# Performance work log

Hardware: AMD Instinct MI355X
Metric: run time of the kernel (lower is better)

The kernel has to match this reference:

```python
import jax, jax.numpy as jnp
import numpy as np

D_MODEL = 2048
NUM_EXPERTS = 64
TOP_K = 2


def setup_inputs() -> dict:
    key = jax.random.key(0)
    kx, kw, kb = jax.random.split(key, 3)
    x = jax.random.normal(kx, (4, 4096, D_MODEL), dtype=jnp.float32)
    # nn.Linear(d_model, num_experts): weight [num_experts, d_model], bias [num_experts]
    bound = 1.0 / np.sqrt(D_MODEL)
    W = jax.random.uniform(kw, (NUM_EXPERTS, D_MODEL), minval=-bound, maxval=bound, dtype=jnp.float32)
    b = jax.random.uniform(kb, (NUM_EXPERTS,), minval=-bound, maxval=bound, dtype=jnp.float32)
    return {"x": x, "W": W, "b": b}


def reference(x, W, b):
    # Eval mode: no noise injection (self.training is False).
    logits = jnp.einsum('bsd,ed->bse', x, W) + b          # [B, S, E]
    raw_weights = jax.nn.softmax(logits, axis=-1)          # [B, S, E]
    top_k_weights, top_k_indices = jax.lax.top_k(raw_weights, TOP_K)  # [B, S, K]
    normalized = top_k_weights / jnp.sum(top_k_weights, axis=-1, keepdims=True)
    return normalized, top_k_indices
```

## Files before the change

kernel.cpp:

```cpp
#include <hip/hip_runtime.h>
#include <math.h>

#define DM 2048
#define NEXP 64
#define NTOK 16384
#define BT 32
#define NW 8
#define KSL (DM / NW)
#define NKS (KSL / 32)
#define NBLK (NTOK / BT)
#define WELEMS (NEXP * DM)

typedef __attribute__((ext_vector_type(8))) short short8;
typedef __attribute__((ext_vector_type(4))) float f32x4;

__device__ __forceinline__ void split3(float f, unsigned short& h,
                                       unsigned short& m, unsigned short& l) {
  unsigned u = __float_as_uint(f);
  unsigned rh = (u + 0x7FFFu + ((u >> 16) & 1u)) >> 16;
  h = (unsigned short)rh;
  float f1 = f - __uint_as_float(rh << 16);
  unsigned u1 = __float_as_uint(f1);
  unsigned rm = (u1 + 0x7FFFu + ((u1 >> 16) & 1u)) >> 16;
  m = (unsigned short)rm;
  float f2 = f1 - __uint_as_float(rm << 16);
  unsigned u2 = __float_as_uint(f2);
  l = (unsigned short)((u2 + 0x7FFFu + ((u2 >> 16) & 1u)) >> 16);
}

__global__ void convw_kernel(const float* __restrict__ W,
                             unsigned short* __restrict__ whi,
                             unsigned short* __restrict__ wmid,
                             unsigned short* __restrict__ wlo) {
  int i = blockIdx.x * 256 + threadIdx.x;
  unsigned short h, m, l;
  split3(W[i], h, m, l);
  whi[i] = h; wmid[i] = m; wlo[i] = l;
}

template <bool USE_WS>
__global__ __launch_bounds__(512, 2)
void router_mfma(const float* __restrict__ x, const float* __restrict__ W,
                 const float* __restrict__ bias,
                 const unsigned short* __restrict__ whi,
                 const unsigned short* __restrict__ wmid,
                 const unsigned short* __restrict__ wlo,
                 float* __restrict__ out) {
  const int lane = threadIdx.x & 63;
  const int wv = threadIdx.x >> 6;
  const int col = lane & 15;
  const int quad = lane >> 4;
  const int tok0 = blockIdx.x * BT;
  const int k0 = wv * KSL;

  __shared__ float part[NW][BT][NEXP];

  f32x4 acc[2][4];
#pragma unroll
  for (int ms = 0; ms < 2; ++ms)
#pragma unroll
    for (int nt = 0; nt < 4; ++nt) acc[ms][nt] = (f32x4){0.f, 0.f, 0.f, 0.f};

  for (int ks = 0; ks < NKS; ++ks) {
    const int k = k0 + ks * 32 + quad * 8;

    short8 ah[2], am[2], al[2];
#pragma unroll
    for (int ms = 0; ms < 2; ++ms) {
      const f32x4* ap = (const f32x4*)(x + (size_t)(tok0 + ms * 16 + col) * DM + k);
      f32x4 a0 = ap[0], a1 = ap[1];
      float av[8] = {a0.x, a0.y, a0.z, a0.w, a1.x, a1.y, a1.z, a1.w};
#pragma unroll
      for (int j = 0; j < 8; ++j) {
        unsigned short h, m, l;
        split3(av[j], h, m, l);
        ah[ms][j] = (short)h; am[ms][j] = (short)m; al[ms][j] = (short)l;
      }
    }

#pragma unroll
    for (int nt = 0; nt < 4; ++nt) {
      short8 bh, bm, bl;
      const size_t widx = (size_t)(nt * 16 + col) * DM + k;
      if (USE_WS) {
        bh = *(const short8*)(whi + widx);
        bm = *(const short8*)(wmid + widx);
        bl = *(const short8*)(wlo + widx);
      } else {
        const f32x4* wp = (const f32x4*)(W + widx);
        f32x4 w0 = wp[0], w1 = wp[1];
        float wvv[8] = {w0.x, w0.y, w0.z, w0.w, w1.x, w1.y, w1.z, w1.w};
#pragma unroll
        for (int j = 0; j < 8; ++j) {
          unsigned short h, m, l;
          split3(wvv[j], h, m, l);
          bh[j] = (short)h; bm[j] = (short)m; bl[j] = (short)l;
        }
      }
#pragma unroll
      for (int ms = 0; ms < 2; ++ms) {
        f32x4 c = acc[ms][nt];
        c = __builtin_amdgcn_mfma_f32_16x16x32_bf16(ah[ms], bh, c, 0, 0, 0);
        c = __builtin_amdgcn_mfma_f32_16x16x32_bf16(ah[ms], bm, c, 0, 0, 0);
        c = __builtin_amdgcn_mfma_f32_16x16x32_bf16(am[ms], bh, c, 0, 0, 0);
        c = __builtin_amdgcn_mfma_f32_16x16x32_bf16(ah[ms], bl, c, 0, 0, 0);
        c = __builtin_amdgcn_mfma_f32_16x16x32_bf16(al[ms], bh, c, 0, 0, 0);
        c = __builtin_amdgcn_mfma_f32_16x16x32_bf16(am[ms], bm, c, 0, 0, 0);
        acc[ms][nt] = c;
      }
    }
  }

#pragma unroll
  for (int ms = 0; ms < 2; ++ms)
#pragma unroll
    for (int nt = 0; nt < 4; ++nt)
#pragma unroll
      for (int r = 0; r < 4; ++r)
        part[wv][ms * 16 + quad * 4 + r][nt * 16 + col] = acc[ms][nt][r];
  __syncthreads();

  const float bl_ = bias[lane];
#pragma unroll
  for (int ti = 0; ti < 4; ++ti) {
    const int t = wv * 4 + ti;
    float v1 = bl_;
#pragma unroll
    for (int p = 0; p < NW; ++p) v1 += part[p][t][lane];
    int i1 = lane;
    float v2 = -INFINITY;
    int i2 = NEXP;
#pragma unroll
    for (int off = 32; off > 0; off >>= 1) {
      float ov1 = __shfl_xor(v1, off, 64);
      int   oi1 = __shfl_xor(i1, off, 64);
      float ov2 = __shfl_xor(v2, off, 64);
      int   oi2 = __shfl_xor(i2, off, 64);
      bool afirst = (v1 > ov1) || (v1 == ov1 && i1 < oi1);
      float w1v = afirst ? v1 : ov1;  int w1i = afirst ? i1 : oi1;
      float c1v = afirst ? v2 : ov2;  int c1i = afirst ? i2 : oi2;
      float c2v = afirst ? ov1 : v1;  int c2i = afirst ? oi1 : i1;
      bool sfirst = (c1v > c2v) || (c1v == c2v && c1i < c2i);
      v1 = w1v; i1 = w1i;
      v2 = sfirst ? c1v : c2v;
      i2 = sfirst ? c1i : c2i;
    }
    if (lane == 0) {
      const float ex = expf(v2 - v1);
      const float den = 1.f + ex;
      const int token = tok0 + t;
      *(float2*)(out + 2 * token) = make_float2(1.f / den, ex / den);
      *(float2*)(out + 2 * NTOK + 2 * token) =
          make_float2((float)i1, (float)i2);
    }
  }
}

extern "C" void kernel_launch(void* const* d_in, const int* in_sizes, int n_in,
                              void* d_out, int out_size, void* d_ws, size_t ws_size,
                              hipStream_t stream) {
  const float* x = (const float*)d_in[0];
  const float* W = (const float*)d_in[1];
  const float* b = (const float*)d_in[2];
  float* out = (float*)d_out;

  const size_t need = 3ull * WELEMS * sizeof(unsigned short);
  if (ws_size >= need) {
    unsigned short* whi = (unsigned short*)d_ws;
    unsigned short* wmid = whi + WELEMS;
    unsigned short* wlo = wmid + WELEMS;
    hipLaunchKernelGGL(convw_kernel, dim3(WELEMS / 256), dim3(256), 0, stream,
                       W, whi, wmid, wlo);
    hipLaunchKernelGGL((router_mfma<true>), dim3(NBLK), dim3(512), 0, stream,
                       x, W, b, whi, wmid, wlo, out);
  } else {
    hipLaunchKernelGGL((router_mfma<false>), dim3(NBLK), dim3(512), 0, stream,
                       x, W, b, nullptr, nullptr, nullptr, out);
  }
}
```

Baseline: 231.8 us.

## Split router into LDS-staged split-K GEMM plus separate top-2 reduce kernel

```diff
diff --git a/kernel.cpp b/kernel.cpp
--- a/kernel.cpp
+++ b/kernel.cpp
@@ -4,129 +4,164 @@
 #define DM 2048
 #define NEXP 64
 #define NTOK 16384
-#define BT 32
-#define NW 8
-#define KSL (DM / NW)
-#define NKS (KSL / 32)
-#define NBLK (NTOK / BT)
-#define WELEMS (NEXP * DM)
+#define NSLICE 8
+#define KSL (DM / NSLICE)
+#define KC 32
+#define NCH (KSL / KC)
+#define MB 128
+#define NBLK1 ((NTOK / MB) * NSLICE)
+#define WFRAG_BYTES (64 * 12 * 1024)
+#define PART_BYTES (NSLICE * NTOK * NEXP * 4)
 
 typedef __attribute__((ext_vector_type(8))) short short8;
 typedef __attribute__((ext_vector_type(4))) float f32x4;
 
-__device__ __forceinline__ void split3(float f, unsigned short& h,
-                                       unsigned short& m, unsigned short& l) {
+__device__ __forceinline__ void async16(void* lds, const void* g) {
+  __builtin_amdgcn_global_load_lds(
+      (const __attribute__((address_space(1))) unsigned int*)g,
+      (__attribute__((address_space(3))) unsigned int*)lds, 16, 0, 0);
+}
+
+__device__ __forceinline__ void split3t(float f, unsigned short& h,
+                                        unsigned short& m, unsigned short& l) {
   unsigned u = __float_as_uint(f);
-  unsigned rh = (u + 0x7FFFu + ((u >> 16) & 1u)) >> 16;
-  h = (unsigned short)rh;
-  float f1 = f - __uint_as_float(rh << 16);
+  h = (unsigned short)(u >> 16);
+  float f1 = f - __uint_as_float(u & 0xFFFF0000u);
   unsigned u1 = __float_as_uint(f1);
-  unsigned rm = (u1 + 0x7FFFu + ((u1 >> 16) & 1u)) >> 16;
-  m = (unsigned short)rm;
-  float f2 = f1 - __uint_as_float(rm << 16);
-  unsigned u2 = __float_as_uint(f2);
-  l = (unsigned short)((u2 + 0x7FFFu + ((u2 >> 16) & 1u)) >> 16);
+  m = (unsigned short)(u1 >> 16);
+  float f2 = f1 - __uint_as_float(u1 & 0xFFFF0000u);
+  l = (unsigned short)(__float_as_uint(f2) >> 16);
+}
+
+__device__ __forceinline__ void split8(const f32x4& a0, const f32x4& a1,
+                                       short8& h, short8& m, short8& l) {
+  float v[8] = {a0[0], a0[1], a0[2], a0[3], a1[0], a1[1], a1[2], a1[3]};
+#pragma unroll
+  for (int j = 0; j < 8; ++j) {
+    unsigned short hh, mm, ll;
+    split3t(v[j], hh, mm, ll);
+    h[j] = (short)hh; m[j] = (short)mm; l[j] = (short)ll;
+  }
 }
 
 __global__ void convw_kernel(const float* __restrict__ W,
-                             unsigned short* __restrict__ whi,
-                             unsigned short* __restrict__ wmid,
-                             unsigned short* __restrict__ wlo) {
-  int i = blockIdx.x * 256 + threadIdx.x;
-  unsigned short h, m, l;
-  split3(W[i], h, m, l);
-  whi[i] = h; wmid[i] = m; wlo[i] = l;
-}
-
-template <bool USE_WS>
-__global__ __launch_bounds__(512, 2)
-void router_mfma(const float* __restrict__ x, const float* __restrict__ W,
-                 const float* __restrict__ bias,
-                 const unsigned short* __restrict__ whi,
-                 const unsigned short* __restrict__ wmid,
-                 const unsigned short* __restrict__ wlo,
-                 float* __restrict__ out) {
+                             unsigned short* __restrict__ wfrag) {
+  const int kg = blockIdx.x;
+  const int lane = threadIdx.x & 63;
+  const int nt = threadIdx.x >> 6;
+  const int e = nt * 16 + (lane & 15);
+  const int kpos = kg * 32 + (lane >> 4) * 8;
+  const f32x4* wp = (const f32x4*)(W + (size_t)e * DM + kpos);
+  f32x4 w0 = wp[0], w1 = wp[1];
+  short8 h, m, l;
+  split8(w0, w1, h, m, l);
+  size_t base = ((size_t)(kg * 12 + nt) * 64 + lane) * 8;
+  *(short8*)(wfrag + base) = h;
+  *(short8*)(wfrag + base + (size_t)4 * 64 * 8) = m;
+  *(short8*)(wfrag + base + (size_t)8 * 64 * 8) = l;
+}
+
+__global__ __launch_bounds__(256, 4)
+void router_gemm(const float* __restrict__ x,
+                 const unsigned short* __restrict__ wfrag,
+                 float* __restrict__ part) {
   const int lane = threadIdx.x & 63;
   const int wv = threadIdx.x >> 6;
   const int col = lane & 15;
   const int quad = lane >> 4;
-  const int tok0 = blockIdx.x * BT;
-  const int k0 = wv * KSL;
-
-  __shared__ float part[NW][BT][NEXP];
+  const int tg = blockIdx.x & ((NTOK / MB) - 1);
+  const int s = blockIdx.x >> 7;
+  const int tok0 = tg * MB;
+
+  __shared__ __align__(16) float xs[MB][KC];
+  __shared__ __align__(16) unsigned short bs[12][64][8];
 
   f32x4 acc[2][4];
 #pragma unroll
-  for (int ms = 0; ms < 2; ++ms)
-#pragma unroll
-    for (int nt = 0; nt < 4; ++nt) acc[ms][nt] = (f32x4){0.f, 0.f, 0.f, 0.f};
-
-  for (int ks = 0; ks < NKS; ++ks) {
-    const int k = k0 + ks * 32 + quad * 8;
+  for (int mt = 0; mt < 2; ++mt)
+#pragma unroll
+    for (int nt = 0; nt < 4; ++nt) acc[mt][nt] = (f32x4){0.f, 0.f, 0.f, 0.f};
+
+  for (int c = 0; c < NCH; ++c) {
+    const int kc = s * KSL + c * KC;
+    const int kg = s * NCH + c;
+
+#pragma unroll
+    for (int i = 0; i < 4; ++i) {
+      const int r = wv * 32 + i * 8;
+      const int tr = r + (lane >> 3);
+      const int unit = (lane & 7) ^ ((lane >> 3) & 7);
+      async16(&xs[r][0],
+              x + (size_t)(tok0 + tr) * DM + kc + unit * 4);
+    }
+#pragma unroll
+    for (int q = 0; q < 3; ++q) {
+      const int m = wv * 3 + q;
+      async16(&bs[m][0][0],
+              wfrag + ((size_t)kg * 12 + m) * 512 + (size_t)lane * 8);
+    }
+    __syncthreads();
 
     short8 ah[2], am[2], al[2];
 #pragma unroll
-    for (int ms = 0; ms < 2; ++ms) {
-      const f32x4* ap = (const f32x4*)(x + (size_t)(tok0 + ms * 16 + col) * DM + k);
-      f32x4 a0 = ap[0], a1 = ap[1];
-      float av[8] = {a0.x, a0.y, a0.z, a0.w, a1.x, a1.y, a1.z, a1.w};
-#pragma unroll
-      for (int j = 0; j < 8; ++j) {
-        unsigned short h, m, l;
-        split3(av[j], h, m, l);
-        ah[ms][j] = (short)h; am[ms][j] = (short)m; al[ms][j] = (short)l;
+    for (int mt = 0; mt < 2; ++mt) {
+      const int row = wv * 32 + mt * 16 + col;
+      const int u0 = (quad * 2) ^ (row & 7);
+      const int u1 = (quad * 2 + 1) ^ (row & 7);
+      f32x4 a0 = *(const f32x4*)&xs[row][u0 * 4];
+      f32x4 a1 = *(const f32x4*)&xs[row][u1 * 4];
+      split8(a0, a1, ah[mt], am[mt], al[mt]);
+    }
+
+#pragma unroll
+    for (int nt = 0; nt < 4; ++nt) {
+      short8 bh = *(const short8*)&bs[nt][lane][0];
+      short8 bm = *(const short8*)&bs[4 + nt][lane][0];
+      short8 bl = *(const short8*)&bs[8 + nt][lane][0];
+#pragma unroll
+      for (int mt = 0; mt < 2; ++mt) {
+        f32x4 cc = acc[mt][nt];
+        cc = __builtin_amdgcn_mfma_f32_16x16x32_bf16(ah[mt], bh, cc, 0, 0, 0);
+        cc = __builtin_amdgcn_mfma_f32_16x16x32_bf16(ah[mt], bm, cc, 0, 0, 0);
+        cc = __builtin_amdgcn_mfma_f32_16x16x32_bf16(am[mt], bh, cc, 0, 0, 0);
+        cc = __builtin_amdgcn_mfma_f32_16x16x32_bf16(ah[mt], bl, cc, 0, 0, 0);
+        cc = __builtin_amdgcn_mfma_f32_16x16x32_bf16(al[mt], bh, cc, 0, 0, 0);
+        cc = __builtin_amdgcn_mfma_f32_16x16x32_bf16(am[mt], bm, cc, 0, 0, 0);
+        acc[mt][nt] = cc;
       }
     }
-
-#pragma unroll
-    for (int nt = 0; nt < 4; ++nt) {
-      short8 bh, bm, bl;
-      const size_t widx = (size_t)(nt * 16 + col) * DM + k;
-      if (USE_WS) {
-        bh = *(const short8*)(whi + widx);
-        bm = *(const short8*)(wmid + widx);
-        bl = *(const short8*)(wlo + widx);
-      } else {
-        const f32x4* wp = (const f32x4*)(W + widx);
-        f32x4 w0 = wp[0], w1 = wp[1];
-        float wvv[8] = {w0.x, w0.y, w0.z, w0.w, w1.x, w1.y, w1.z, w1.w};
-#pragma unroll
-        for (int j = 0; j < 8; ++j) {
-          unsigned short h, m, l;
-          split3(wvv[j], h, m, l);
-          bh[j] = (short)h; bm[j] = (short)m; bl[j] = (short)l;
-        }
+    __syncthreads();
+  }
+
+#pragma unroll
+  for (int mt = 0; mt < 2; ++mt)
+#pragma unroll
+    for (int nt = 0; nt < 4; ++nt)
+#pragma unroll
+      for (int r = 0; r < 4; ++r) {
+        const int token = tok0 + wv * 32 + mt * 16 + quad * 4 + r;
+        const int e = nt * 16 + col;
+        part[((size_t)s * NTOK + token) * NEXP + e] = acc[mt][nt][r];
       }
-#pragma unroll
-      for (int ms = 0; ms < 2; ++ms) {
-        f32x4 c = acc[ms][nt];
-        c = __builtin_amdgcn_mfma_f32_16x16x32_bf16(ah[ms], bh, c, 0, 0, 0);
-        c = __builtin_amdgcn_mfma_f32_16x16x32_bf16(ah[ms], bm, c, 0, 0, 0);
-        c = __builtin_amdgcn_mfma_f32_16x16x32_bf16(am[ms], bh, c, 0, 0, 0);
-        c = __builtin_amdgcn_mfma_f32_16x16x32_bf16(ah[ms], bl, c, 0, 0, 0);
-        c = __builtin_amdgcn_mfma_f32_16x16x32_bf16(al[ms], bh, c, 0, 0, 0);
-        c = __builtin_amdgcn_mfma_f32_16x16x32_bf16(am[ms], bm, c, 0, 0, 0);
-        acc[ms][nt] = c;
-      }
-    }
-  }
-
-#pragma unroll
-  for (int ms = 0; ms < 2; ++ms)
-#pragma unroll
-    for (int nt = 0; nt < 4; ++nt)
-#pragma unroll
-      for (int r = 0; r < 4; ++r)
-        part[wv][ms * 16 + quad * 4 + r][nt * 16 + col] = acc[ms][nt][r];
-  __syncthreads();
-
-  const float bl_ = bias[lane];
-#pragma unroll
-  for (int ti = 0; ti < 4; ++ti) {
-    const int t = wv * 4 + ti;
-    float v1 = bl_;
-#pragma unroll
-    for (int p = 0; p < NW; ++p) v1 += part[p][t][lane];
+}
+
+__global__ __launch_bounds__(256, 8)
+void router_reduce(const float* __restrict__ part,
+                   const float* __restrict__ bias, float* __restrict__ out) {
+  const int lane = threadIdx.x & 63;
+  const int wv = threadIdx.x >> 6;
+  const float bl = bias[lane];
+  const int t0 = blockIdx.x * 8 + wv * 2;
+#pragma unroll
+  for (int tt = 0; tt < 2; ++tt) {
+    const int t = t0 + tt;
+    float p[NSLICE];
+#pragma unroll
+    for (int sl = 0; sl < NSLICE; ++sl)
+      p[sl] = part[((size_t)sl * NTOK + t) * NEXP + lane];
+    float v1 = bl;
+#pragma unroll
+    for (int sl = 0; sl < NSLICE; ++sl) v1 += p[sl];
     int i1 = lane;
     float v2 = -INFINITY;
     int i2 = NEXP;
@@ -148,6 +183,94 @@
     if (lane == 0) {
       const float ex = expf(v2 - v1);
       const float den = 1.f + ex;
+      *(float2*)(out + 2 * t) = make_float2(1.f / den, ex / den);
+      *(float2*)(out + 2 * NTOK + 2 * t) = make_float2((float)i1, (float)i2);
+    }
+  }
+}
+
+__global__ __launch_bounds__(512, 2)
+void router_fb(const float* __restrict__ x, const float* __restrict__ W,
+               const float* __restrict__ bias, float* __restrict__ out) {
+  const int lane = threadIdx.x & 63;
+  const int wv = threadIdx.x >> 6;
+  const int col = lane & 15;
+  const int quad = lane >> 4;
+  const int tok0 = blockIdx.x * 32;
+  const int k0 = wv * 256;
+
+  __shared__ float part[8][32][68];
+
+  f32x4 acc[2][4];
+#pragma unroll
+  for (int ms = 0; ms < 2; ++ms)
+#pragma unroll
+    for (int nt = 0; nt < 4; ++nt) acc[ms][nt] = (f32x4){0.f, 0.f, 0.f, 0.f};
+
+  for (int ks = 0; ks < 8; ++ks) {
+    const int k = k0 + ks * 32 + quad * 8;
+    short8 ah[2], am2[2], al2[2];
+#pragma unroll
+    for (int ms = 0; ms < 2; ++ms) {
+      const f32x4* ap = (const f32x4*)(x + (size_t)(tok0 + ms * 16 + col) * DM + k);
+      f32x4 a0 = ap[0], a1 = ap[1];
+      split8(a0, a1, ah[ms], am2[ms], al2[ms]);
+    }
+#pragma unroll
+    for (int nt = 0; nt < 4; ++nt) {
+      short8 bh, bm, bl;
+      const f32x4* wp = (const f32x4*)(W + (size_t)(nt * 16 + col) * DM + k);
+      f32x4 w0 = wp[0], w1 = wp[1];
+      split8(w0, w1, bh, bm, bl);
+#pragma unroll
+      for (int ms = 0; ms < 2; ++ms) {
+        f32x4 cc = acc[ms][nt];
+        cc = __builtin_amdgcn_mfma_f32_16x16x32_bf16(ah[ms], bh, cc, 0, 0, 0);
+        cc = __builtin_amdgcn_mfma_f32_16x16x32_bf16(ah[ms], bm, cc, 0, 0, 0);
+        cc = __builtin_amdgcn_mfma_f32_16x16x32_bf16(am2[ms], bh, cc, 0, 0, 0);
+        cc = __builtin_amdgcn_mfma_f32_16x16x32_bf16(ah[ms], bl, cc, 0, 0, 0);
+        cc = __builtin_amdgcn_mfma_f32_16x16x32_bf16(al2[ms], bh, cc, 0, 0, 0);
+        cc = __builtin_amdgcn_mfma_f32_16x16x32_bf16(am2[ms], bm, cc, 0, 0, 0);
+        acc[ms][nt] = cc;
+      }
+    }
+  }
+#pragma unroll
+  for (int ms = 0; ms < 2; ++ms)
+#pragma unroll
+    for (int nt = 0; nt < 4; ++nt)
+#pragma unroll
+      for (int r = 0; r < 4; ++r)
+        part[wv][ms * 16 + quad * 4 + r][nt * 16 + col] = acc[ms][nt][r];
+  __syncthreads();
+  const float bl_ = bias[lane];
+#pragma unroll
+  for (int ti = 0; ti < 4; ++ti) {
+    const int t = wv * 4 + ti;
+    float v1 = bl_;
+#pragma unroll
+    for (int p = 0; p < 8; ++p) v1 += part[p][t][lane];
+    int i1 = lane;
+    float v2 = -INFINITY;
+    int i2 = NEXP;
+#pragma unroll
+    for (int off = 32; off > 0; off >>= 1) {
+      float ov1 = __shfl_xor(v1, off, 64);
+      int   oi1 = __shfl_xor(i1, off, 64);
+      float ov2 = __shfl_xor(v2, off, 64);
+      int   oi2 = __shfl_xor(i2, off, 64);
+      bool afirst = (v1 > ov1) || (v1 == ov1 && i1 < oi1);
+      float w1v = afirst ? v1 : ov1;  int w1i = afirst ? i1 : oi1;
+      float c1v = afirst ? v2 : ov2;  int c1i = afirst ? i2 : oi2;
+      float c2v = afirst ? ov1 : v1;  int c2i = afirst ? oi1 : i1;
+      bool sfirst = (c1v > c2v) || (c1v == c2v && c1i < c2i);
+      v1 = w1v; i1 = w1i;
+      v2 = sfirst ? c1v : c2v;
+      i2 = sfirst ? c1i : c2i;
+    }
+    if (lane == 0) {
+      const float ex = expf(v2 - v1);
+      const float den = 1.f + ex;
       const int token = tok0 + t;
       *(float2*)(out + 2 * token) = make_float2(1.f / den, ex / den);
       *(float2*)(out + 2 * NTOK + 2 * token) =
@@ -164,17 +287,17 @@
   const float* b = (const float*)d_in[2];
   float* out = (float*)d_out;
 
-  const size_t need = 3ull * WELEMS * sizeof(unsigned short);
+  const size_t need = (size_t)WFRAG_BYTES + (size_t)PART_BYTES;
   if (ws_size >= need) {
-    unsigned short* whi = (unsigned short*)d_ws;
-    unsigned short* wmid = whi + WELEMS;
-    unsigned short* wlo = wmid + WELEMS;
-    hipLaunchKernelGGL(convw_kernel, dim3(WELEMS / 256), dim3(256), 0, stream,
-                       W, whi, wmid, wlo);
-    hipLaunchKernelGGL((router_mfma<true>), dim3(NBLK), dim3(512), 0, stream,
-                       x, W, b, whi, wmid, wlo, out);
+    unsigned short* wfrag = (unsigned short*)d_ws;
+    float* part = (float*)((char*)d_ws + WFRAG_BYTES);
+    hipLaunchKernelGGL(convw_kernel, dim3(64), dim3(256), 0, stream, W, wfrag);
+    hipLaunchKernelGGL(router_gemm, dim3(NBLK1), dim3(256), 0, stream,
+                       x, wfrag, part);
+    hipLaunchKernelGGL(router_reduce, dim3(NTOK / 8), dim3(256), 0, stream,
+                       part, b, out);
   } else {
-    hipLaunchKernelGGL((router_mfma<false>), dim3(NBLK), dim3(512), 0, stream,
-                       x, W, b, nullptr, nullptr, nullptr, out);
-  }
-}
+    hipLaunchKernelGGL(router_fb, dim3(NTOK / 32), dim3(512), 0, stream,
+                       x, W, b, out);
+  }
+}
```

Measured after the change: 217.3 us. -6.3%, faster.
